# Kernel optimization log

Hardware: AMD Instinct MI355X
Metric: run time of the kernel (lower is better)

Reference implementation:

```python
import jax, jax.numpy as jnp
import numpy as np

N = 100000   # nodes per type
E = 1600000  # edges per edge type
F = 128      # input feature dim
C = 256      # out_channels


def setup_inputs() -> dict:
    key = jax.random.key(0)
    ks = iter(jax.random.split(key, 32))
    d = {}
    d["x_A"] = jax.random.normal(next(ks), (N, F), jnp.float32)
    d["x_B"] = jax.random.normal(next(ks), (N, F), jnp.float32)
    d["h_A"] = jax.random.normal(next(ks), (N, F), jnp.float32)
    d["h_B"] = jax.random.normal(next(ks), (N, F), jnp.float32)
    d["eidx_ab"] = jax.random.randint(next(ks), (2, E), 0, N, jnp.int32)
    d["eidx_ba"] = jax.random.randint(next(ks), (2, E), 0, N, jnp.int32)
    # per-node-type input linears (bias=False) and output biases
    d["lin_A"] = jax.random.normal(next(ks), (F, C), jnp.float32) / np.sqrt(F)
    d["lin_B"] = jax.random.normal(next(ks), (F, C), jnp.float32) / np.sqrt(F)
    d["bias_A"] = jax.random.uniform(next(ks), (C,), jnp.float32)
    d["bias_B"] = jax.random.uniform(next(ks), (C,), jnp.float32)
    # SAGEConv params: per layer (0,1) x per edge type (ab: A->B, ba: B->A)
    #   Wl: neighbor (lin_l) weight [C,C], bl: lin_l bias [C], Wr: root (lin_r) weight [C,C]
    for l in range(2):
        for et in ("ab", "ba"):
            d[f"Wl_{et}{l}"] = jax.random.normal(next(ks), (C, C), jnp.float32) / np.sqrt(C)
            d[f"bl_{et}{l}"] = jnp.zeros((C,), jnp.float32)
            d[f"Wr_{et}{l}"] = jax.random.normal(next(ks), (C, C), jnp.float32) / np.sqrt(C)
    return d


def _sage(x_src, x_dst, eidx, Wl, bl, Wr):
    # PyG SAGEConv (mean aggr): lin_l(mean_{j->i} x_src[j]) + bias + lin_r(x_dst[i])
    src, dst = eidx[0], eidx[1]
    n_dst = x_dst.shape[0]
    agg = jax.ops.segment_sum(x_src[src], dst, num_segments=n_dst)      # [N_dst, C]
    cnt = jax.ops.segment_sum(jnp.ones_like(dst, dtype=x_src.dtype), dst,
                              num_segments=n_dst)                       # [N_dst]
    mean = agg / jnp.maximum(cnt, 1.0)[:, None]
    return mean @ Wl + bl + x_dst @ Wr


def reference(x_A, x_B, h_A, h_B, eidx_ab, eidx_ba,
              lin_A, lin_B, bias_A, bias_B,
              Wl_ab0, bl_ab0, Wr_ab0, Wl_ba0, bl_ba0, Wr_ba0,
              Wl_ab1, bl_ab1, Wr_ab1, Wl_ba1, bl_ba1, Wr_ba1):
    # per-type input projection
    oA = x_A @ lin_A
    oB = x_B @ lin_B
    # layer 0: A gets messages via B->A, B via A->B (one edge type per dst -> no hetero sum)
    nA = _sage(oB, oA, eidx_ba, Wl_ba0, bl_ba0, Wr_ba0)
    nB = _sage(oA, oB, eidx_ab, Wl_ab0, bl_ab0, Wr_ab0)
    oA, oB = nA, nB
    # layer 1
    nA = _sage(oB, oA, eidx_ba, Wl_ba1, bl_ba1, Wr_ba1)
    nB = _sage(oA, oB, eidx_ab, Wl_ab1, bl_ab1, Wr_ab1)
    oA, oB = nA, nB
    # per-type bias + sigmoid gate
    gA = jax.nn.sigmoid(bias_A + oA)
    gB = jax.nn.sigmoid(bias_B + oB)
    return jnp.stack([gA, gB])  # [2, N, C]
```

## Files before the change

### kernel.cpp

```cpp
#include <hip/hip_runtime.h>
#include <math.h>

#define NN 100000
#define EE 1600000
#define NBU 782
#define NCH 196
#define CHUNK 8192

typedef short s16x8 __attribute__((ext_vector_type(8)));
typedef float f32x4 __attribute__((ext_vector_type(4)));

union FragU { uint4 u; s16x8 s; };

__device__ __forceinline__ unsigned short f2bf(float x) {
    unsigned int u = __float_as_uint(x);
    u = (u + 0x7fff + ((u >> 16) & 1)) >> 16;
    return (unsigned short)u;
}
__device__ __forceinline__ float bf2f(unsigned short b) {
    return __uint_as_float(((unsigned int)b) << 16);
}
__device__ __forceinline__ float bflo(unsigned int u) { return __uint_as_float(u << 16); }
__device__ __forceinline__ float bfhi(unsigned int u) { return __uint_as_float(u & 0xffff0000u); }

__device__ __forceinline__ void gload16(const unsigned short* g, unsigned short* l) {
    __builtin_amdgcn_global_load_lds(
        (const __attribute__((address_space(1))) unsigned int*)g,
        (__attribute__((address_space(3))) unsigned int*)l, 16, 0, 0);
}

template<int K1, int K2, int MODE>
__global__ __launch_bounds__(256)
void gemm_mfma(const unsigned short* __restrict__ A1,
               const unsigned short* __restrict__ A2,
               const unsigned short* __restrict__ BT,
               const float* __restrict__ bl, const float* __restrict__ b2,
               void* __restrict__ Cout, int M)
{
    constexpr int KT = K1 + K2;
    __shared__ __align__(16) unsigned short As[128 * 32];
    __shared__ __align__(16) unsigned short Bs[128 * 32];

    const int tid  = threadIdx.x;
    const int w    = tid >> 6, lane = tid & 63;
    const int l15  = lane & 15, g = lane >> 4;
    const int m0   = blockIdx.x * 128;
    const int n0   = blockIdx.y * 128;
    const int wm   = (w >> 1) * 64, wn = (w & 1) * 64;

    f32x4 acc[4][4];
#pragma unroll
    for (int i = 0; i < 4; i++)
#pragma unroll
        for (int j = 0; j < 4; j++) { acc[i][j][0]=0.f; acc[i][j][1]=0.f; acc[i][j][2]=0.f; acc[i][j][3]=0.f; }

    for (int k0 = 0; k0 < KT; k0 += 32) {
        const unsigned short* Ap; int astr, kloc;
        if (K1 > 0 && k0 < K1) { Ap = A1; astr = K1; kloc = k0; }
        else                   { Ap = A2; astr = K2; kloc = k0 - K1; }

#pragma unroll
        for (int c = 0; c < 2; c++) {
            const int chunk = ((w * 2 + c) << 6) + lane;
            const int row = chunk >> 2, kc = chunk & 3;
            int rg = m0 + row; if (rg > M - 1) rg = M - 1;
            gload16(Ap + (size_t)rg * astr + kloc + kc * 8, As + (w * 2 + c) * 512);
            gload16(BT + (size_t)(n0 + row) * KT + k0 + kc * 8, Bs + (w * 2 + c) * 512);
        }
        __syncthreads();

        FragU a[4], b[4];
#pragma unroll
        for (int i = 0; i < 4; i++) {
            a[i].u = *(const uint4*)(As + (wm + i * 16 + l15) * 32 + g * 8);
            b[i].u = *(const uint4*)(Bs + (wn + i * 16 + l15) * 32 + g * 8);
        }
#pragma unroll
        for (int i = 0; i < 4; i++)
#pragma unroll
            for (int j = 0; j < 4; j++)
                acc[i][j] = __builtin_amdgcn_mfma_f32_16x16x32_bf16(a[i].s, b[j].s, acc[i][j], 0, 0, 0);
        __syncthreads();
    }

    float badd[4];
#pragma unroll
    for (int j = 0; j < 4; j++) {
        const int col = n0 + wn + j * 16 + l15;
        badd[j] = bl ? bl[col] : 0.0f;
        if (MODE == 1) badd[j] += b2[col];
    }
#pragma unroll
    for (int i = 0; i < 4; i++) {
#pragma unroll
        for (int r = 0; r < 4; r++) {
            const int rowg = m0 + wm + i * 16 + g * 4 + r;
            if (rowg < M) {
#pragma unroll
                for (int j = 0; j < 4; j++) {
                    const int col = n0 + wn + j * 16 + l15;
                    float t = acc[i][j][r] + badd[j];
                    if (MODE == 1) {
                        t = 1.0f / (1.0f + __expf(-t));
                        ((float*)Cout)[(size_t)rowg * 256 + col] = t;
                    } else {
                        ((unsigned short*)Cout)[(size_t)rowg * 256 + col] = f2bf(t);
                    }
                }
            }
        }
    }
}

__device__ __forceinline__ int wave_incl_scan(int v, int lane)
{
#pragma unroll
    for (int off = 1; off < 64; off <<= 1) {
        int t = __shfl_up(v, off, 64);
        if (lane >= off) v += t;
    }
    return v;
}

__global__ __launch_bounds__(256)
void p1_count(const int* __restrict__ dba, const int* __restrict__ dab,
              int* __restrict__ cnt)
{
    __shared__ int h[NBU];
    const int y = blockIdx.y, b = blockIdx.x;
    for (int i = threadIdx.x; i < NBU; i += 256) h[i] = 0;
    __syncthreads();
    const int* D = y ? dab : dba;
    const int base = b * CHUNK;
    for (int i = threadIdx.x; i < CHUNK; i += 256) {
        const int e = base + i;
        if (e < EE) atomicAdd(&h[D[e] >> 7], 1);
    }
    __syncthreads();
    for (int i = threadIdx.x; i < NBU; i += 256)
        cnt[(y * NCH + b) * NBU + i] = h[i];
}

__global__ __launch_bounds__(1024)
void p2_scan(const int* __restrict__ cnt, int* __restrict__ baseG)
{
    __shared__ int tot[2 * NBU];
    const int tid = threadIdx.x;
    for (int i = tid; i < 2 * NBU; i += 1024) {
        const int y = i / NBU, u = i - y * NBU;
        int s = 0;
#pragma unroll 4
        for (int b = 0; b < NCH; b++) s += cnt[(y * NCH + b) * NBU + u];
        tot[i] = s;
    }
    __syncthreads();
    const int lane = tid & 63, wid = tid >> 6;
    if (wid < 2) {
        int run = 0;
        for (int c = 0; c < NBU; c += 64) {
            const int ui = c + lane;
            const int v = (ui < NBU) ? tot[wid * NBU + ui] : 0;
            const int incl = wave_incl_scan(v, lane);
            if (ui < NBU) baseG[wid * (NBU + 1) + ui] = run + incl - v;
            run += __shfl(incl, 63, 64);
        }
        if (lane == 0) baseG[wid * (NBU + 1) + NBU] = run;
    }
}

__global__ __launch_bounds__(256)
void p2b_off(const int* __restrict__ cnt, const int* __restrict__ baseG,
             int* __restrict__ blockOff)
{
    const int i = blockIdx.x * 256 + threadIdx.x;
    if (i >= 2 * NBU) return;
    const int y = i / NBU, u = i - y * NBU;
    int run = baseG[y * (NBU + 1) + u];
#pragma unroll 4
    for (int b = 0; b < NCH; b++) {
        blockOff[(y * NCH + b) * NBU + u] = run;
        run += cnt[(y * NCH + b) * NBU + u];
    }
}

__global__ __launch_bounds__(256)
void p3_scatter(const int* __restrict__ sba, const int* __restrict__ dba,
                const int* __restrict__ sab, const int* __restrict__ dab,
                const int* __restrict__ blockOff, int* __restrict__ stage)
{
    __shared__ int cur[NBU];
    const int y = blockIdx.y, b = blockIdx.x;
    for (int i = threadIdx.x; i < NBU; i += 256)
        cur[i] = blockOff[(y * NCH + b) * NBU + i];
    __syncthreads();
    const int* S = y ? sab : sba;
    const int* D = y ? dab : dba;
    int* st = stage + (size_t)y * EE;
    const int base = b * CHUNK;
    for (int i = threadIdx.x; i < CHUNK; i += 256) {
        const int e = base + i;
        if (e < EE) {
            const int d = D[e], s = S[e];
            const int p = atomicAdd(&cur[d >> 7], 1);
            __builtin_nontemporal_store((s << 7) | (d & 127), &st[p]);
        }
    }
}

__global__ __launch_bounds__(256)
void p4_fine(const int* __restrict__ baseG, const int* __restrict__ stage,
             int* __restrict__ rowptr, int* __restrict__ ssrc)
{
    __shared__ int out[8192];
    __shared__ int hist[128], off[128], curs[128];
    const int y = blockIdx.y, u = blockIdx.x;
    const int t = threadIdx.x;
    const int base = baseG[y * (NBU + 1) + u];
    const int cnt_ = baseG[y * (NBU + 1) + u + 1] - base;
    const int n0 = u * 128;
    if (t < 128) hist[t] = 0;
    __syncthreads();
    const int* st = stage + (size_t)y * EE + base;
    for (int i = t; i < cnt_; i += 256) atomicAdd(&hist[st[i] & 127], 1);
    __syncthreads();
    if (t < 64) {
        const int v0 = hist[t];
        const int i0 = wave_incl_scan(v0, t);
        off[t] = i0 - v0;
        const int tot0 = __shfl(i0, 63, 64);
        const int v1 = hist[64 + t];
        const int i1 = wave_incl_scan(v1, t);
        off[64 + t] = tot0 + i1 - v1;
    }
    __syncthreads();
    if (t < 128) {
        curs[t] = off[t];
        const int node = n0 + t;
        if (node < NN) rowptr[y * (NN + 1) + node] = base + off[t];
    }
    if (t == 0 && u == 0) rowptr[y * (NN + 1) + NN] = EE;
    __syncthreads();
    for (int i = t; i < cnt_; i += 256) {
        const int w = st[i];
        const int p = atomicAdd(&curs[w & 127], 1);
        if (p < 8192) out[p] = w >> 7;
    }
    __syncthreads();
    int* dp = ssrc + (size_t)y * EE + base;
    const int lim = (cnt_ < 8192) ? cnt_ : 8192;
    for (int i = t; i < lim; i += 256)
        __builtin_nontemporal_store(out[i], &dp[i]);
}

__global__ __launch_bounds__(128)
void agg_bf(const unsigned short* __restrict__ feat, const int* __restrict__ rowptr,
            const int* __restrict__ ssrc, unsigned short* __restrict__ out)
{
    __shared__ float red[32][8];
    const int node = blockIdx.x;
    const int t = threadIdx.x;
    const int slot = t >> 5;
    const int c = t & 31;
    const int beg = rowptr[node], end = rowptr[node + 1];
    const int deg = end - beg;

    float a0=0.f,a1=0.f,a2=0.f,a3=0.f,a4=0.f,a5=0.f,a6=0.f,a7=0.f;
    for (int i = beg + slot; i < end; i += 4) {
        const uint4 v = *(const uint4*)(feat + ((size_t)ssrc[i] << 8) + c * 8);
        a0 += bflo(v.x); a1 += bfhi(v.x);
        a2 += bflo(v.y); a3 += bfhi(v.y);
        a4 += bflo(v.z); a5 += bfhi(v.z);
        a6 += bflo(v.w); a7 += bfhi(v.w);
    }
    a0 += __shfl_xor(a0, 32, 64); a1 += __shfl_xor(a1, 32, 64);
    a2 += __shfl_xor(a2, 32, 64); a3 += __shfl_xor(a3, 32, 64);
    a4 += __shfl_xor(a4, 32, 64); a5 += __shfl_xor(a5, 32, 64);
    a6 += __shfl_xor(a6, 32, 64); a7 += __shfl_xor(a7, 32, 64);
    if (t >= 64 && t < 96) {
        red[c][0]=a0; red[c][1]=a1; red[c][2]=a2; red[c][3]=a3;
        red[c][4]=a4; red[c][5]=a5; red[c][6]=a6; red[c][7]=a7;
    }
    __syncthreads();
    if (t < 32) {
        a0 += red[c][0]; a1 += red[c][1]; a2 += red[c][2]; a3 += red[c][3];
        a4 += red[c][4]; a5 += red[c][5]; a6 += red[c][6]; a7 += red[c][7];
        const float inv = 1.0f / fmaxf((float)deg, 1.0f);
        uint4 o;
        o.x = (unsigned int)f2bf(a0 * inv) | ((unsigned int)f2bf(a1 * inv) << 16);
        o.y = (unsigned int)f2bf(a2 * inv) | ((unsigned int)f2bf(a3 * inv) << 16);
        o.z = (unsigned int)f2bf(a4 * inv) | ((unsigned int)f2bf(a5 * inv) << 16);
        o.w = (unsigned int)f2bf(a6 * inv) | ((unsigned int)f2bf(a7 * inv) << 16);
        *(uint4*)(out + ((size_t)node << 8) + c * 8) = o;
    }
}

__global__ __launch_bounds__(256)
void f2bf4_kernel(const float* __restrict__ in, unsigned short* __restrict__ out, int n4)
{
    const int i = blockIdx.x * 256 + threadIdx.x;
    if (i < n4) {
        const float4 v = ((const float4*)in)[i];
        ushort4 o;
        o.x = f2bf(v.x); o.y = f2bf(v.y); o.z = f2bf(v.z); o.w = f2bf(v.w);
        ((ushort4*)out)[i] = o;
    }
}

__global__ __launch_bounds__(256)
void wt_kernel(const float* __restrict__ W, unsigned short* __restrict__ WT,
               int K, int KT, int koff)
{
    const int idx = blockIdx.x * 256 + threadIdx.x;
    if (idx < K * 256) {
        const int k = idx >> 8, n = idx & 255;
        WT[(size_t)n * KT + koff + k] = f2bf(W[(size_t)k * 256 + n]);
    }
}

extern "C" void kernel_launch(void* const* d_in, const int* in_sizes, int n_in,
                              void* d_out, int out_size, void* d_ws, size_t ws_size,
                              hipStream_t stream)
{
    const float* x_A    = (const float*)d_in[0];
    const float* x_B    = (const float*)d_in[1];
    const int*   e_ab   = (const int*)d_in[4];
    const int*   e_ba   = (const int*)d_in[5];
    const float* lin_A  = (const float*)d_in[6];
    const float* lin_B  = (const float*)d_in[7];
    const float* bias_A = (const float*)d_in[8];
    const float* bias_B = (const float*)d_in[9];
    const float* Wl_ab0 = (const float*)d_in[10]; const float* bl_ab0 = (const float*)d_in[11]; const float* Wr_ab0 = (const float*)d_in[12];
    const float* Wl_ba0 = (const float*)d_in[13]; const float* bl_ba0 = (const float*)d_in[14]; const float* Wr_ba0 = (const float*)d_in[15];
    const float* Wl_ab1 = (const float*)d_in[16]; const float* bl_ab1 = (const float*)d_in[17]; const float* Wr_ab1 = (const float*)d_in[18];
    const float* Wl_ba1 = (const float*)d_in[19]; const float* bl_ba1 = (const float*)d_in[20]; const float* Wr_ba1 = (const float*)d_in[21];

    float* gA = (float*)d_out;
    float* gB = gA + (size_t)NN * 256;

    const size_t HALF = (size_t)NN * 128;
    const size_t FULL = (size_t)NN * 256;
    unsigned short* xb    = (unsigned short*)d_ws;
    unsigned short* xbA   = xb;
    unsigned short* xbB   = xb + HALF;
    unsigned short* l0A   = xb;
    unsigned short* projA = xb + FULL;
    unsigned short* l0B   = projA;
    unsigned short* projB = projA + FULL;
    unsigned short* aggb  = projB + FULL;
    unsigned short* linAT = aggb + FULL;
    unsigned short* linBT = linAT + 256 * 128;
    unsigned short* WTba0 = linBT + 256 * 128;
    unsigned short* WTab0 = WTba0 + 256 * 512;
    unsigned short* WTba1 = WTab0 + 256 * 512;
    unsigned short* WTab1 = WTba1 + 256 * 512;
    int* ssrc2   = (int*)(WTab1 + 256 * 512);
    int* rowptr2 = ssrc2 + 2 * (size_t)EE;

    int* stage    = (int*)aggb;
    int* cnt      = stage + 2 * (size_t)EE;
    int* blockOff = cnt + 2 * NCH * NBU;
    int* baseG    = blockOff + 2 * NCH * NBU;

    int* ssrc_ba   = ssrc2;
    int* ssrc_ab   = ssrc2 + EE;
    int* rowptr_ba = rowptr2;
    int* rowptr_ab = rowptr2 + (NN + 1);

    const int* src_ab = e_ab;  const int* dst_ab = e_ab + EE;
    const int* src_ba = e_ba;  const int* dst_ba = e_ba + EE;

    const dim3 gg((NN + 127) / 128, 2);
    const dim3 gCh(NCH, 2);
    const dim3 gBu(NBU, 2);

    p1_count<<<gCh, 256, 0, stream>>>(dst_ba, dst_ab, cnt);
    p2_scan<<<1, 1024, 0, stream>>>(cnt, baseG);
    p2b_off<<<(2 * NBU + 255) / 256, 256, 0, stream>>>(cnt, baseG, blockOff);
    p3_scatter<<<gCh, 256, 0, stream>>>(src_ba, dst_ba, src_ab, dst_ab, blockOff, stage);
    p4_fine<<<gBu, 256, 0, stream>>>(baseG, stage, rowptr2, ssrc2);

    f2bf4_kernel<<<(int)(HALF / 4 + 255) / 256, 256, 0, stream>>>(x_A, xbA, (int)(HALF / 4));
    f2bf4_kernel<<<(int)(HALF / 4 + 255) / 256, 256, 0, stream>>>(x_B, xbB, (int)(HALF / 4));
    wt_kernel<<<128, 256, 0, stream>>>(lin_A, linAT, 128, 128, 0);
    wt_kernel<<<128, 256, 0, stream>>>(lin_B, linBT, 128, 128, 0);
    wt_kernel<<<256, 256, 0, stream>>>(Wl_ba0, WTba0, 256, 512, 0);
    wt_kernel<<<256, 256, 0, stream>>>(Wr_ba0, WTba0, 256, 512, 256);
    wt_kernel<<<256, 256, 0, stream>>>(Wl_ab0, WTab0, 256, 512, 0);
    wt_kernel<<<256, 256, 0, stream>>>(Wr_ab0, WTab0, 256, 512, 256);
    wt_kernel<<<256, 256, 0, stream>>>(Wl_ba1, WTba1, 256, 512, 0);
    wt_kernel<<<256, 256, 0, stream>>>(Wr_ba1, WTba1, 256, 512, 256);
    wt_kernel<<<256, 256, 0, stream>>>(Wl_ab1, WTab1, 256, 512, 0);
    wt_kernel<<<256, 256, 0, stream>>>(Wr_ab1, WTab1, 256, 512, 256);

    gemm_mfma<0, 128, 0><<<gg, 256, 0, stream>>>(nullptr, xbA, linAT, nullptr, nullptr, projA, NN);
    gemm_mfma<0, 128, 0><<<gg, 256, 0, stream>>>(nullptr, xbB, linBT, nullptr, nullptr, projB, NN);

    agg_bf<<<NN, 128, 0, stream>>>(projB, rowptr_ba, ssrc_ba, aggb);
    gemm_mfma<256, 256, 0><<<gg, 256, 0, stream>>>(aggb, projA, WTba0, bl_ba0, nullptr, l0A, NN);
    agg_bf<<<NN, 128, 0, stream>>>(projA, rowptr_ab, ssrc_ab, aggb);
    gemm_mfma<256, 256, 0><<<gg, 256, 0, stream>>>(aggb, projB, WTab0, bl_ab0, nullptr, l0B, NN);

    agg_bf<<<NN, 128, 0, stream>>>(l0B, rowptr_ba, ssrc_ba, aggb);
    gemm_mfma<256, 256, 1><<<gg, 256, 0, stream>>>(aggb, l0A, WTba1, bl_ba1, bias_A, gA, NN);
    agg_bf<<<NN, 128, 0, stream>>>(l0A, rowptr_ab, ssrc_ab, aggb);
    gemm_mfma<256, 256, 1><<<gg, 256, 0, stream>>>(aggb, l0B, WTab1, bl_ab1, bias_B, gB, NN);
}
```

Measured before the change: 1.300 ms.

## Fuse neighbor mean aggregation into SAGE GEMM and batch both edge types per launch

Adds a fused kernel in which each block gathers and averages neighbor features for 64 destination nodes straight into shared memory as bf16, then runs the MFMA GEMM over the concatenated [mean, root] inputs with bias and optional sigmoid. Both edge types are handled in one launch through blockIdx.y. This removes the aggregated-feature buffer round trip through global memory and cuts the per-layer launches from four to one. In exchange it uses a 64-row tile with 48KB of LDS, which may lower occupancy and GEMM efficiency, and each thread walks a whole neighbor list serially instead of spreading it over several slots. The workspace buffer for l0B is moved so both directions can be written without aliasing their inputs.

```diff
diff --git a/kernel.cpp b/kernel.cpp
--- a/kernel.cpp
+++ b/kernel.cpp
@@ -6,6 +6,7 @@
 #define NBU 782
 #define NCH 196
 #define CHUNK 8192
+#define MB64 1563
 
 typedef short s16x8 __attribute__((ext_vector_type(8)));
 typedef float f32x4 __attribute__((ext_vector_type(4)));
@@ -112,6 +113,153 @@
     }
 }
 
+template<int MODE>
+__global__ __launch_bounds__(256)
+void fused_sage(const int* __restrict__ rowptr2, const int* __restrict__ ssrc2,
+                const unsigned short* __restrict__ fsrc0, const unsigned short* __restrict__ fsrc1,
+                const unsigned short* __restrict__ fdst0, const unsigned short* __restrict__ fdst1,
+                const unsigned short* __restrict__ BT0, const unsigned short* __restrict__ BT1,
+                const float* __restrict__ bl0, const float* __restrict__ bl1,
+                const float* __restrict__ b20, const float* __restrict__ b21,
+                void* __restrict__ out0, void* __restrict__ out1)
+{
+    __shared__ __align__(16) unsigned short Abuf[64 * 256];
+    __shared__ __align__(16) unsigned short Bs[256 * 32];
+    __shared__ __align__(16) unsigned short As2[64 * 32];
+
+    const int y   = blockIdx.y;
+    const int m0  = blockIdx.x * 64;
+    const int tid = threadIdx.x;
+
+    const int* rowptr = rowptr2 + y * (NN + 1);
+    const int* ssrc   = ssrc2 + (size_t)y * EE;
+    const unsigned short* fsrc = y ? fsrc1 : fsrc0;
+    const unsigned short* fdst = y ? fdst1 : fdst0;
+    const unsigned short* BT   = y ? BT1 : BT0;
+    const float* bl = y ? bl1 : bl0;
+    const float* b2 = y ? b21 : b20;
+    void* out       = y ? out1 : out0;
+
+    {
+        const int grp = tid >> 5, c = tid & 31;
+        for (int q = 0; q < 8; q++) {
+            const int r = grp * 8 + q;
+            const int node = m0 + r;
+            uint4 o = make_uint4(0u, 0u, 0u, 0u);
+            if (node < NN) {
+                const int beg = rowptr[node], end = rowptr[node + 1];
+                float a0=0.f,a1=0.f,a2=0.f,a3=0.f,a4=0.f,a5=0.f,a6=0.f,a7=0.f;
+                int i = beg;
+                for (; i + 4 <= end; i += 4) {
+                    const int s0 = ssrc[i], s1 = ssrc[i+1], s2 = ssrc[i+2], s3 = ssrc[i+3];
+                    const uint4 v0 = *(const uint4*)(fsrc + ((size_t)s0 << 8) + c * 8);
+                    const uint4 v1 = *(const uint4*)(fsrc + ((size_t)s1 << 8) + c * 8);
+                    const uint4 v2 = *(const uint4*)(fsrc + ((size_t)s2 << 8) + c * 8);
+                    const uint4 v3 = *(const uint4*)(fsrc + ((size_t)s3 << 8) + c * 8);
+                    a0 += bflo(v0.x)+bflo(v1.x)+bflo(v2.x)+bflo(v3.x);
+                    a1 += bfhi(v0.x)+bfhi(v1.x)+bfhi(v2.x)+bfhi(v3.x);
+                    a2 += bflo(v0.y)+bflo(v1.y)+bflo(v2.y)+bflo(v3.y);
+                    a3 += bfhi(v0.y)+bfhi(v1.y)+bfhi(v2.y)+bfhi(v3.y);
+                    a4 += bflo(v0.z)+bflo(v1.z)+bflo(v2.z)+bflo(v3.z);
+                    a5 += bfhi(v0.z)+bfhi(v1.z)+bfhi(v2.z)+bfhi(v3.z);
+                    a6 += bflo(v0.w)+bflo(v1.w)+bflo(v2.w)+bflo(v3.w);
+                    a7 += bfhi(v0.w)+bfhi(v1.w)+bfhi(v2.w)+bfhi(v3.w);
+                }
+                for (; i < end; ++i) {
+                    const uint4 v = *(const uint4*)(fsrc + ((size_t)ssrc[i] << 8) + c * 8);
+                    a0 += bflo(v.x); a1 += bfhi(v.x);
+                    a2 += bflo(v.y); a3 += bfhi(v.y);
+                    a4 += bflo(v.z); a5 += bfhi(v.z);
+                    a6 += bflo(v.w); a7 += bfhi(v.w);
+                }
+                const float inv = 1.0f / fmaxf((float)(end - beg), 1.0f);
+                o.x = (unsigned int)f2bf(a0*inv) | ((unsigned int)f2bf(a1*inv) << 16);
+                o.y = (unsigned int)f2bf(a2*inv) | ((unsigned int)f2bf(a3*inv) << 16);
+                o.z = (unsigned int)f2bf(a4*inv) | ((unsigned int)f2bf(a5*inv) << 16);
+                o.w = (unsigned int)f2bf(a6*inv) | ((unsigned int)f2bf(a7*inv) << 16);
+            }
+            const int idx = r * 256 + ((c * 8) ^ ((r & 7) << 3));
+            *(uint4*)(Abuf + idx) = o;
+        }
+    }
+
+    const int w = tid >> 6, lane = tid & 63;
+    const int l15 = lane & 15, g = lane >> 4;
+    const int wn = w * 64;
+
+    f32x4 acc[4][4];
+#pragma unroll
+    for (int i = 0; i < 4; i++)
+#pragma unroll
+        for (int j = 0; j < 4; j++) { acc[i][j][0]=0.f; acc[i][j][1]=0.f; acc[i][j][2]=0.f; acc[i][j][3]=0.f; }
+
+    for (int k0 = 0; k0 < 512; k0 += 32) {
+#pragma unroll
+        for (int cc = 0; cc < 4; cc++) {
+            const int chunk = cc * 256 + w * 64 + lane;
+            const int row = chunk >> 2, kc = chunk & 3;
+            gload16(BT + (size_t)row * 512 + k0 + kc * 8, Bs + (cc * 256 + w * 64) * 8);
+        }
+        if (k0 >= 256) {
+            const int chunk = w * 64 + lane;
+            const int row = chunk >> 2, kc = chunk & 3;
+            int rg = m0 + row; if (rg > NN - 1) rg = NN - 1;
+            gload16(fdst + ((size_t)rg << 8) + (k0 - 256) + kc * 8, As2 + w * 512);
+        }
+        __syncthreads();
+
+        FragU a[4], b[4];
+        if (k0 < 256) {
+#pragma unroll
+            for (int i = 0; i < 4; i++) {
+                const int row = i * 16 + l15;
+                a[i].u = *(const uint4*)(Abuf + row * 256 + ((k0 + g * 8) ^ ((row & 7) << 3)));
+            }
+        } else {
+#pragma unroll
+            for (int i = 0; i < 4; i++)
+                a[i].u = *(const uint4*)(As2 + (i * 16 + l15) * 32 + g * 8);
+        }
+#pragma unroll
+        for (int j = 0; j < 4; j++)
+            b[j].u = *(const uint4*)(Bs + (wn + j * 16 + l15) * 32 + g * 8);
+#pragma unroll
+        for (int i = 0; i < 4; i++)
+#pragma unroll
+            for (int j = 0; j < 4; j++)
+                acc[i][j] = __builtin_amdgcn_mfma_f32_16x16x32_bf16(a[i].s, b[j].s, acc[i][j], 0, 0, 0);
+        __syncthreads();
+    }
+
+    float badd[4];
+#pragma unroll
+    for (int j = 0; j < 4; j++) {
+        const int col = wn + j * 16 + l15;
+        badd[j] = bl[col];
+        if (MODE == 1) badd[j] += b2[col];
+    }
+#pragma unroll
+    for (int i = 0; i < 4; i++) {
+#pragma unroll
+        for (int r = 0; r < 4; r++) {
+            const int rowg = m0 + i * 16 + g * 4 + r;
+            if (rowg < NN) {
+#pragma unroll
+                for (int j = 0; j < 4; j++) {
+                    const int col = wn + j * 16 + l15;
+                    float t = acc[i][j][r] + badd[j];
+                    if (MODE == 1) {
+                        t = 1.0f / (1.0f + __expf(-t));
+                        ((float*)out)[(size_t)rowg * 256 + col] = t;
+                    } else {
+                        ((unsigned short*)out)[(size_t)rowg * 256 + col] = f2bf(t);
+                    }
+                }
+            }
+        }
+    }
+}
+
 __device__ __forceinline__ int wave_incl_scan(int v, int lane)
 {
 #pragma unroll
@@ -250,48 +398,6 @@
     const int lim = (cnt_ < 8192) ? cnt_ : 8192;
     for (int i = t; i < lim; i += 256)
         __builtin_nontemporal_store(out[i], &dp[i]);
-}
-
-__global__ __launch_bounds__(128)
-void agg_bf(const unsigned short* __restrict__ feat, const int* __restrict__ rowptr,
-            const int* __restrict__ ssrc, unsigned short* __restrict__ out)
-{
-    __shared__ float red[32][8];
-    const int node = blockIdx.x;
-    const int t = threadIdx.x;
-    const int slot = t >> 5;
-    const int c = t & 31;
-    const int beg = rowptr[node], end = rowptr[node + 1];
-    const int deg = end - beg;
-
-    float a0=0.f,a1=0.f,a2=0.f,a3=0.f,a4=0.f,a5=0.f,a6=0.f,a7=0.f;
-    for (int i = beg + slot; i < end; i += 4) {
-        const uint4 v = *(const uint4*)(feat + ((size_t)ssrc[i] << 8) + c * 8);
-        a0 += bflo(v.x); a1 += bfhi(v.x);
-        a2 += bflo(v.y); a3 += bfhi(v.y);
-        a4 += bflo(v.z); a5 += bfhi(v.z);
-        a6 += bflo(v.w); a7 += bfhi(v.w);
-    }
-    a0 += __shfl_xor(a0, 32, 64); a1 += __shfl_xor(a1, 32, 64);
-    a2 += __shfl_xor(a2, 32, 64); a3 += __shfl_xor(a3, 32, 64);
-    a4 += __shfl_xor(a4, 32, 64); a5 += __shfl_xor(a5, 32, 64);
-    a6 += __shfl_xor(a6, 32, 64); a7 += __shfl_xor(a7, 32, 64);
-    if (t >= 64 && t < 96) {
-        red[c][0]=a0; red[c][1]=a1; red[c][2]=a2; red[c][3]=a3;
-        red[c][4]=a4; red[c][5]=a5; red[c][6]=a6; red[c][7]=a7;
-    }
-    __syncthreads();
-    if (t < 32) {
-        a0 += red[c][0]; a1 += red[c][1]; a2 += red[c][2]; a3 += red[c][3];
-        a4 += red[c][4]; a5 += red[c][5]; a6 += red[c][6]; a7 += red[c][7];
-        const float inv = 1.0f / fmaxf((float)deg, 1.0f);
-        uint4 o;
-        o.x = (unsigned int)f2bf(a0 * inv) | ((unsigned int)f2bf(a1 * inv) << 16);
-        o.y = (unsigned int)f2bf(a2 * inv) | ((unsigned int)f2bf(a3 * inv) << 16);
-        o.z = (unsigned int)f2bf(a4 * inv) | ((unsigned int)f2bf(a5 * inv) << 16);
-        o.w = (unsigned int)f2bf(a6 * inv) | ((unsigned int)f2bf(a7 * inv) << 16);
-        *(uint4*)(out + ((size_t)node << 8) + c * 8) = o;
-    }
 }
 
 __global__ __launch_bounds__(256)
@@ -344,9 +450,9 @@
     unsigned short* xbB   = xb + HALF;
     unsigned short* l0A   = xb;
     unsigned short* projA = xb + FULL;
-    unsigned short* l0B   = projA;
     unsigned short* projB = projA + FULL;
     unsigned short* aggb  = projB + FULL;
+    unsigned short* l0B   = aggb;
     unsigned short* linAT = aggb + FULL;
     unsigned short* linBT = linAT + 256 * 128;
     unsigned short* WTba0 = linBT + 256 * 128;
@@ -361,17 +467,13 @@
     int* blockOff = cnt + 2 * NCH * NBU;
     int* baseG    = blockOff + 2 * NCH * NBU;
 
-    int* ssrc_ba   = ssrc2;
-    int* ssrc_ab   = ssrc2 + EE;
-    int* rowptr_ba = rowptr2;
-    int* rowptr_ab = rowptr2 + (NN + 1);
-
     const int* src_ab = e_ab;  const int* dst_ab = e_ab + EE;
     const int* src_ba = e_ba;  const int* dst_ba = e_ba + EE;
 
     const dim3 gg((NN + 127) / 128, 2);
     const dim3 gCh(NCH, 2);
     const dim3 gBu(NBU, 2);
+    const dim3 gF(MB64, 2);
 
     p1_count<<<gCh, 256, 0, stream>>>(dst_ba, dst_ab, cnt);
     p2_scan<<<1, 1024, 0, stream>>>(cnt, baseG);
@@ -395,13 +497,13 @@
     gemm_mfma<0, 128, 0><<<gg, 256, 0, stream>>>(nullptr, xbA, linAT, nullptr, nullptr, projA, NN);
     gemm_mfma<0, 128, 0><<<gg, 256, 0, stream>>>(nullptr, xbB, linBT, nullptr, nullptr, projB, NN);
 
-    agg_bf<<<NN, 128, 0, stream>>>(projB, rowptr_ba, ssrc_ba, aggb);
-    gemm_mfma<256, 256, 0><<<gg, 256, 0, stream>>>(aggb, projA, WTba0, bl_ba0, nullptr, l0A, NN);
-    agg_bf<<<NN, 128, 0, stream>>>(projA, rowptr_ab, ssrc_ab, aggb);
-    gemm_mfma<256, 256, 0><<<gg, 256, 0, stream>>>(aggb, projB, WTab0, bl_ab0, nullptr, l0B, NN);
-
-    agg_bf<<<NN, 128, 0, stream>>>(l0B, rowptr_ba, ssrc_ba, aggb);
-    gemm_mfma<256, 256, 1><<<gg, 256, 0, stream>>>(aggb, l0A, WTba1, bl_ba1, bias_A, gA, NN);
-    agg_bf<<<NN, 128, 0, stream>>>(l0A, rowptr_ab, ssrc_ab, aggb);
-    gemm_mfma<256, 256, 1><<<gg, 256, 0, stream>>>(aggb, l0B, WTab1, bl_ab1, bias_B, gB, NN);
-}
+    fused_sage<0><<<gF, 256, 0, stream>>>(rowptr2, ssrc2,
+        projB, projA,
+        projA, projB,
+        WTba0, WTab0, bl_ba0, bl_ab0, nullptr, nullptr, l0A, l0B);
+
+    fused_sage<1><<<gF, 256, 0, stream>>>(rowptr2, ssrc2,
+        l0B, l0A,
+        l0A, l0B,
+        WTba1, WTab1, bl_ba1, bl_ab1, bias_A, bias_B, gA, gB);
+}
```

After: 1.257 ms. -3.3%, faster.
